# Optimization experiments

Hardware: AMD Instinct MI355X
Metric: run time of the kernel (lower is better)

The kernel has to match this reference:

```python
import jax, jax.numpy as jnp
import numpy as np

WS = 7            # window size
N = WS * WS       # tokens per window (49)
DIM = 128
HEADS = 4
HEAD_DIM = DIM // HEADS
SCALE = HEAD_DIM ** -0.5
NW = 64           # number of windows (mask leading dim)
B_WIN = 4096      # B * nW


def _relative_position_index():
    coords = np.stack(np.meshgrid(np.arange(WS), np.arange(WS), indexing='ij'))  # (2,WS,WS)
    cf = coords.reshape(2, -1)                       # (2, N)
    rel = cf[:, :, None] - cf[:, None, :]            # (2, N, N)
    rel = rel.transpose(1, 2, 0).copy()              # (N, N, 2)
    rel[..., 0] += WS - 1
    rel[..., 1] += WS - 1
    rel[..., 0] *= 2 * WS - 1
    return rel.sum(-1)                               # (N, N) int

REL_IDX = jnp.asarray(_relative_position_index())


def setup_inputs() -> dict:
    key = jax.random.key(0)
    ks = jax.random.split(key, 7)
    return {
        'x': jax.random.normal(ks[0], (B_WIN, N, DIM), dtype=jnp.float32),
        'mask': jax.random.normal(ks[1], (NW, N, N), dtype=jnp.float32),
        'qkv_w': jax.random.normal(ks[2], (3 * DIM, DIM), dtype=jnp.float32) * 0.02,
        'qkv_b': jax.random.normal(ks[3], (3 * DIM,), dtype=jnp.float32) * 0.02,
        'proj_w': jax.random.normal(ks[4], (DIM, DIM), dtype=jnp.float32) * 0.02,
        'proj_b': jax.random.normal(ks[5], (DIM,), dtype=jnp.float32) * 0.02,
        'bias_table': jax.random.normal(ks[6], ((2 * WS - 1) ** 2, HEADS), dtype=jnp.float32) * 0.02,
    }


def reference(x, mask, qkv_w, qkv_b, proj_w, proj_b, bias_table):
    B_, n, C = x.shape
    # qkv projection: (B_, N, 3C) -> (3, B_, H, N, hd)
    qkv = (x @ qkv_w.T + qkv_b).reshape(B_, n, 3, HEADS, HEAD_DIM)
    qkv = jnp.transpose(qkv, (2, 0, 3, 1, 4))
    q, k, v = qkv[0], qkv[1], qkv[2]
    # scaled scores: (B_, H, N, N)
    attn = jnp.einsum('bhnd,bhmd->bhnm', q * SCALE, k)
    # gathered relative position bias: (N, N, H) -> (H, N, N)
    rel_bias = jnp.transpose(bias_table[REL_IDX], (2, 0, 1))
    attn = attn + rel_bias[None]
    # shifted-window mask: broadcast over batch groups and heads
    nW = mask.shape[0]
    attn = attn.reshape(B_ // nW, nW, HEADS, n, n) + mask[None, :, None]
    attn = attn.reshape(B_, HEADS, n, n)
    attn = jax.nn.softmax(attn, axis=-1)
    out = jnp.einsum('bhnm,bhmd->bhnd', attn, v)
    out = jnp.transpose(out, (0, 2, 1, 3)).reshape(B_, n, C)
    return out @ proj_w.T + proj_b
```

## Files before the change

kernel.cpp:

```cpp
#include <hip/hip_runtime.h>

#define QK_SCALE 0.17677669529663687f

typedef __attribute__((ext_vector_type(8))) short bf16x8;
typedef __attribute__((ext_vector_type(4))) short bf16x4;
typedef __attribute__((ext_vector_type(4))) float floatx4;

__device__ __forceinline__ unsigned short f2bf(float f) {
    unsigned int u = __float_as_uint(f);
    u += 0x7fffu + ((u >> 16) & 1u);
    return (unsigned short)(u >> 16);
}

__device__ __forceinline__ bf16x8 ld8_2x4(const short* p) {
    union { bf16x8 v8; bf16x4 v4[2]; } u;
    u.v4[0] = *(const bf16x4*)p;
    u.v4[1] = *(const bf16x4*)(p + 4);
    return u.v8;
}

__global__ __launch_bounds__(256) void prep_kernel(
    const float* __restrict__ qkv_w, const float* __restrict__ proj_w,
    const float* __restrict__ bias_table, const float* __restrict__ mask,
    unsigned short* __restrict__ wbf, float* __restrict__ cm)
{
    int g = blockIdx.x * 256 + threadIdx.x;
    if (g < 49152) {
        wbf[g] = f2bf(qkv_w[g]);
    } else if (g < 65536) {
        wbf[g] = f2bf(proj_w[g - 49152]);
    } else if (g < 680192) {
        int t = g - 65536;
        int j = t % 49; int t2 = t / 49;
        int i = t2 % 49; int t3 = t2 / 49;
        int h = t3 & 3;  int wn = t3 >> 2;
        int idx = (i / 7 - j / 7 + 6) * 13 + (i % 7 - j % 7 + 6);
        cm[t] = mask[wn * 2401 + i * 49 + j] + bias_table[idx * 4 + h];
    }
}

__global__ __launch_bounds__(256, 3) void winattn_mfma(
    const float* __restrict__ x,
    const float* __restrict__ qkv_b,
    const float* __restrict__ proj_b,
    const unsigned short* __restrict__ wbf,
    const float* __restrict__ cm,
    float* __restrict__ out)
{
    __shared__ __align__(16) short smem[27136];

    const int tid  = threadIdx.x;
    const int lane = tid & 63;
    const int lid  = lane & 15;
    const int quad = lane >> 4;
    const int h    = tid >> 6;
    const int b    = blockIdx.x;
    const int w    = b & 63;
    const int hq   = h * 6784;

    {
        const float4* xg = (const float4*)(x + (size_t)b * 6272);
        for (int i = tid; i < 1568; i += 256) {
            int n = i >> 5, c4 = i & 31;
            float4 v = xg[i];
            ushort4 u;
            u.x = f2bf(v.x); u.y = f2bf(v.y); u.z = f2bf(v.z); u.w = f2bf(v.w);
            *(ushort4*)&smem[n * 136 + c4 * 4] = u;
        }
        ushort4 z; z.x = 0; z.y = 0; z.z = 0; z.w = 0;
        for (int i = tid; i < 510; i += 256)
            *(ushort4*)&smem[49 * 136 + i * 4] = z;
    }
    __syncthreads();

    bf16x8 ax[4][4];
    #pragma unroll
    for (int mt = 0; mt < 4; ++mt)
        #pragma unroll
        for (int kb = 0; kb < 4; ++kb)
            ax[mt][kb] = *(const bf16x8*)&smem[(mt * 16 + lid) * 136 + kb * 32 + quad * 8];
    __syncthreads();

    const floatx4 z4 = {0.f, 0.f, 0.f, 0.f};

    #pragma unroll
    for (int t = 0; t < 6; ++t) {
        const int cb = (t < 2) ? (h * 32 + t * 16)
                     : (t < 4) ? (128 + h * 32 + (t - 2) * 16)
                               : (256 + h * 32 + (t - 4) * 16);
        const unsigned short* wr = wbf + (size_t)(cb + lid) * 128 + quad * 8;
        floatx4 acc[4] = {z4, z4, z4, z4};
        #pragma unroll
        for (int kb = 0; kb < 4; ++kb) {
            bf16x8 bw = *(const bf16x8*)(wr + kb * 32);
            #pragma unroll
            for (int mt = 0; mt < 4; ++mt)
                acc[mt] = __builtin_amdgcn_mfma_f32_16x16x32_bf16(ax[mt][kb], bw, acc[mt], 0, 0, 0);
        }
        const float bias = qkv_b[cb + lid];
        #pragma unroll
        for (int mt = 0; mt < 4; ++mt) {
            #pragma unroll
            for (int r = 0; r < 4; ++r) {
                const int row = mt * 16 + quad * 4 + r;
                const float v = acc[mt][r] + bias;
                if (t < 2) {
                    smem[hq + row * 36 + t * 16 + lid] = (short)f2bf(v * QK_SCALE);
                } else if (t < 4) {
                    smem[hq + 2304 + row * 36 + (t - 2) * 16 + lid] = (short)f2bf(v);
                } else {
                    smem[hq + 4608 + ((t - 4) * 16 + lid) * 68 + row] = (short)f2bf(v);
                }
            }
        }
    }

    bf16x8 aq[4], bk[4];
    #pragma unroll
    for (int mt = 0; mt < 4; ++mt)
        aq[mt] = ld8_2x4(&smem[hq + (mt * 16 + lid) * 36 + quad * 8]);
    #pragma unroll
    for (int nt = 0; nt < 4; ++nt)
        bk[nt] = ld8_2x4(&smem[hq + 2304 + (nt * 16 + lid) * 36 + quad * 8]);

    floatx4 sacc[4][4];
    #pragma unroll
    for (int mt = 0; mt < 4; ++mt)
        #pragma unroll
        for (int nt = 0; nt < 4; ++nt)
            sacc[mt][nt] = __builtin_amdgcn_mfma_f32_16x16x32_bf16(aq[mt], bk[nt], z4, 0, 0, 0);

    float invs[4][4];
    const float* cmb = cm + (size_t)(w * 4 + h) * 2401;
    #pragma unroll
    for (int mt = 0; mt < 4; ++mt) {
        #pragma unroll
        for (int r = 0; r < 4; ++r) {
            const int row  = mt * 16 + quad * 4 + r;
            const int rowc = (row < 49) ? row : 48;
            float sv[4];
            #pragma unroll
            for (int nt = 0; nt < 4; ++nt) {
                const int col  = nt * 16 + lid;
                const int colc = (col < 49) ? col : 48;
                float val = sacc[mt][nt][r] + cmb[rowc * 49 + colc];
                sv[nt] = (col < 49) ? val : -1e30f;
            }
            float mx = fmaxf(fmaxf(sv[0], sv[1]), fmaxf(sv[2], sv[3]));
            #pragma unroll
            for (int d = 1; d < 16; d <<= 1) mx = fmaxf(mx, __shfl_xor(mx, d));
            float sum = 0.f;
            #pragma unroll
            for (int nt = 0; nt < 4; ++nt) { float p = __expf(sv[nt] - mx); sv[nt] = p; sum += p; }
            #pragma unroll
            for (int d = 1; d < 16; d <<= 1) sum += __shfl_xor(sum, d);
            invs[mt][r] = 1.f / sum;
            #pragma unroll
            for (int nt = 0; nt < 4; ++nt)
                smem[hq + row * 72 + nt * 16 + lid] = (short)f2bf(sv[nt]);
        }
    }

    bf16x8 bv[2][2];
    #pragma unroll
    for (int nt2 = 0; nt2 < 2; ++nt2)
        #pragma unroll
        for (int kb2 = 0; kb2 < 2; ++kb2)
            bv[nt2][kb2] = ld8_2x4(&smem[hq + 4608 + (nt2 * 16 + lid) * 68 + kb2 * 32 + quad * 8]);

    floatx4 oacc[4][2] = {{z4, z4}, {z4, z4}, {z4, z4}, {z4, z4}};
    #pragma unroll
    for (int mt = 0; mt < 4; ++mt) {
        #pragma unroll
        for (int kb2 = 0; kb2 < 2; ++kb2) {
            bf16x8 ap = *(const bf16x8*)&smem[hq + (mt * 16 + lid) * 72 + kb2 * 32 + quad * 8];
            #pragma unroll
            for (int nt2 = 0; nt2 < 2; ++nt2)
                oacc[mt][nt2] = __builtin_amdgcn_mfma_f32_16x16x32_bf16(ap, bv[nt2][kb2], oacc[mt][nt2], 0, 0, 0);
        }
    }

    __syncthreads();

    #pragma unroll
    for (int mt = 0; mt < 4; ++mt)
        #pragma unroll
        for (int nt2 = 0; nt2 < 2; ++nt2)
            #pragma unroll
            for (int r = 0; r < 4; ++r) {
                const int row = mt * 16 + quad * 4 + r;
                smem[row * 136 + h * 32 + nt2 * 16 + lid] =
                    (short)f2bf(oacc[mt][nt2][r] * invs[mt][r]);
            }
    __syncthreads();

    bf16x8 aa[4][4];
    #pragma unroll
    for (int mt = 0; mt < 4; ++mt)
        #pragma unroll
        for (int kb = 0; kb < 4; ++kb)
            aa[mt][kb] = *(const bf16x8*)&smem[(mt * 16 + lid) * 136 + kb * 32 + quad * 8];

    float* outb = out + (size_t)b * 6272;
    #pragma unroll
    for (int nt = 0; nt < 2; ++nt) {
        const int cb = h * 32 + nt * 16;
        const unsigned short* wr = wbf + 49152 + (size_t)(cb + lid) * 128 + quad * 8;
        floatx4 acc[4] = {z4, z4, z4, z4};
        #pragma unroll
        for (int kb = 0; kb < 4; ++kb) {
            bf16x8 bw = *(const bf16x8*)(wr + kb * 32);
            #pragma unroll
            for (int mt = 0; mt < 4; ++mt)
                acc[mt] = __builtin_amdgcn_mfma_f32_16x16x32_bf16(aa[mt][kb], bw, acc[mt], 0, 0, 0);
        }
        const float pb = proj_b[cb + lid];
        #pragma unroll
        for (int mt = 0; mt < 4; ++mt)
            #pragma unroll
            for (int r = 0; r < 4; ++r) {
                const int row = mt * 16 + quad * 4 + r;
                if (row < 49)
                    outb[row * 128 + cb + lid] = acc[mt][r] + pb;
            }
    }
}

extern "C" void kernel_launch(void* const* d_in, const int* in_sizes, int n_in,
                              void* d_out, int out_size, void* d_ws, size_t ws_size,
                              hipStream_t stream) {
    (void)in_sizes; (void)n_in; (void)out_size; (void)ws_size;
    const float* x          = (const float*)d_in[0];
    const float* mask       = (const float*)d_in[1];
    const float* qkv_w      = (const float*)d_in[2];
    const float* qkv_b      = (const float*)d_in[3];
    const float* proj_w     = (const float*)d_in[4];
    const float* proj_b     = (const float*)d_in[5];
    const float* bias_table = (const float*)d_in[6];

    unsigned short* wbf = (unsigned short*)d_ws;
    float* cm           = (float*)((char*)d_ws + 131072);

    prep_kernel<<<2657, 256, 0, stream>>>(qkv_w, proj_w, bias_table, mask, wbf, cm);
    winattn_mfma<<<4096, 256, 0, stream>>>(x, qkv_b, proj_b, wbf, cm, (float*)d_out);
}
```

Measured before the change: 300.5 us.

## Repack combined mask-bias into padded float4 layout and prefetch it per row tile

The prep kernel now writes the combined mask and relative-position bias in a layout padded to 64 columns, pre-filled with -1e30 for the padding, and interleaved so each lane reads its four column values as one float4. The attention kernel prefetches the next row tile of these values before doing the softmax on the current one, removing scalar clamped gathers and the column select. Shared-memory row strides are also tightened (36 to 34, 72 to 68), shrinking LDS use, which may allow more resident blocks. In exchange the prep kernel writes a somewhat larger table, and the odd strides need 2-element LDS loads.

```diff
diff --git a/kernel.cpp b/kernel.cpp
--- a/kernel.cpp
+++ b/kernel.cpp
@@ -4,6 +4,7 @@
 
 typedef __attribute__((ext_vector_type(8))) short bf16x8;
 typedef __attribute__((ext_vector_type(4))) short bf16x4;
+typedef __attribute__((ext_vector_type(2))) short bf16x2;
 typedef __attribute__((ext_vector_type(4))) float floatx4;
 
 __device__ __forceinline__ unsigned short f2bf(float f) {
@@ -19,23 +20,43 @@
     return u.v8;
 }
 
+__device__ __forceinline__ bf16x8 ld8_4x2(const short* p) {
+    union { bf16x8 v8; bf16x2 v2[4]; } u;
+    u.v2[0] = *(const bf16x2*)p;
+    u.v2[1] = *(const bf16x2*)(p + 2);
+    u.v2[2] = *(const bf16x2*)(p + 4);
+    u.v2[3] = *(const bf16x2*)(p + 6);
+    return u.v8;
+}
+
 __global__ __launch_bounds__(256) void prep_kernel(
     const float* __restrict__ qkv_w, const float* __restrict__ proj_w,
     const float* __restrict__ bias_table, const float* __restrict__ mask,
-    unsigned short* __restrict__ wbf, float* __restrict__ cm)
+    unsigned short* __restrict__ wbf, float* __restrict__ cm2)
 {
     int g = blockIdx.x * 256 + threadIdx.x;
     if (g < 49152) {
         wbf[g] = f2bf(qkv_w[g]);
     } else if (g < 65536) {
         wbf[g] = f2bf(proj_w[g - 49152]);
-    } else if (g < 680192) {
+    } else if (g < 868352) {
         int t = g - 65536;
-        int j = t % 49; int t2 = t / 49;
-        int i = t2 % 49; int t3 = t2 / 49;
-        int h = t3 & 3;  int wn = t3 >> 2;
-        int idx = (i / 7 - j / 7 + 6) * 13 + (i % 7 - j % 7 + 6);
-        cm[t] = mask[wn * 2401 + i * 49 + j] + bias_table[idx * 4 + h];
+        int nt  = t & 3;
+        int lid = (t >> 2) & 15;
+        int t2  = t >> 6;
+        int row = t2 % 49;
+        int wh  = t2 / 49;
+        int h   = wh & 3;
+        int w   = wh >> 2;
+        int col = nt * 16 + lid;
+        float v;
+        if (col < 49) {
+            int idx = (row / 7 - col / 7 + 6) * 13 + (row % 7 - col % 7 + 6);
+            v = mask[w * 2401 + row * 49 + col] + bias_table[idx * 4 + h];
+        } else {
+            v = -1e30f;
+        }
+        cm2[t] = v;
     }
 }
 
@@ -44,10 +65,10 @@
     const float* __restrict__ qkv_b,
     const float* __restrict__ proj_b,
     const unsigned short* __restrict__ wbf,
-    const float* __restrict__ cm,
+    const float* __restrict__ cm2,
     float* __restrict__ out)
 {
-    __shared__ __align__(16) short smem[27136];
+    __shared__ __align__(16) short smem[26112];
 
     const int tid  = threadIdx.x;
     const int lane = tid & 63;
@@ -56,7 +77,7 @@
     const int h    = tid >> 6;
     const int b    = blockIdx.x;
     const int w    = b & 63;
-    const int hq   = h * 6784;
+    const int hq   = h * 6528;
 
     {
         const float4* xg = (const float4*)(x + (size_t)b * 6272);
@@ -105,23 +126,29 @@
                 const int row = mt * 16 + quad * 4 + r;
                 const float v = acc[mt][r] + bias;
                 if (t < 2) {
-                    smem[hq + row * 36 + t * 16 + lid] = (short)f2bf(v * QK_SCALE);
+                    smem[hq + row * 34 + t * 16 + lid] = (short)f2bf(v * QK_SCALE);
                 } else if (t < 4) {
-                    smem[hq + 2304 + row * 36 + (t - 2) * 16 + lid] = (short)f2bf(v);
+                    smem[hq + 2176 + row * 34 + (t - 2) * 16 + lid] = (short)f2bf(v);
                 } else {
-                    smem[hq + 4608 + ((t - 4) * 16 + lid) * 68 + row] = (short)f2bf(v);
+                    smem[hq + 4352 + ((t - 4) * 16 + lid) * 68 + row] = (short)f2bf(v);
                 }
             }
         }
     }
 
+    const float4* cm2b = (const float4*)cm2 + ((size_t)(w * 4 + h) * 49) * 16 + lid;
+    float4 cmv[4][4];
+    #pragma unroll
+    for (int r = 0; r < 4; ++r)
+        cmv[0][r] = cm2b[(quad * 4 + r) * 16];
+
     bf16x8 aq[4], bk[4];
     #pragma unroll
     for (int mt = 0; mt < 4; ++mt)
-        aq[mt] = ld8_2x4(&smem[hq + (mt * 16 + lid) * 36 + quad * 8]);
+        aq[mt] = ld8_4x2(&smem[hq + (mt * 16 + lid) * 34 + quad * 8]);
     #pragma unroll
     for (int nt = 0; nt < 4; ++nt)
-        bk[nt] = ld8_2x4(&smem[hq + 2304 + (nt * 16 + lid) * 36 + quad * 8]);
+        bk[nt] = ld8_4x2(&smem[hq + 2176 + (nt * 16 + lid) * 34 + quad * 8]);
 
     floatx4 sacc[4][4];
     #pragma unroll
@@ -131,21 +158,23 @@
             sacc[mt][nt] = __builtin_amdgcn_mfma_f32_16x16x32_bf16(aq[mt], bk[nt], z4, 0, 0, 0);
 
     float invs[4][4];
-    const float* cmb = cm + (size_t)(w * 4 + h) * 2401;
     #pragma unroll
     for (int mt = 0; mt < 4; ++mt) {
+        if (mt < 3) {
+            #pragma unroll
+            for (int r = 0; r < 4; ++r) {
+                const int row  = (mt + 1) * 16 + quad * 4 + r;
+                const int rowc = (row < 49) ? row : 48;
+                cmv[mt + 1][r] = cm2b[rowc * 16];
+            }
+        }
         #pragma unroll
         for (int r = 0; r < 4; ++r) {
-            const int row  = mt * 16 + quad * 4 + r;
-            const int rowc = (row < 49) ? row : 48;
+            const int row = mt * 16 + quad * 4 + r;
             float sv[4];
             #pragma unroll
-            for (int nt = 0; nt < 4; ++nt) {
-                const int col  = nt * 16 + lid;
-                const int colc = (col < 49) ? col : 48;
-                float val = sacc[mt][nt][r] + cmb[rowc * 49 + colc];
-                sv[nt] = (col < 49) ? val : -1e30f;
-            }
+            for (int nt = 0; nt < 4; ++nt)
+                sv[nt] = sacc[mt][nt][r] + cmv[mt][r][nt];
             float mx = fmaxf(fmaxf(sv[0], sv[1]), fmaxf(sv[2], sv[3]));
             #pragma unroll
             for (int d = 1; d < 16; d <<= 1) mx = fmaxf(mx, __shfl_xor(mx, d));
@@ -157,7 +186,7 @@
             invs[mt][r] = 1.f / sum;
             #pragma unroll
             for (int nt = 0; nt < 4; ++nt)
-                smem[hq + row * 72 + nt * 16 + lid] = (short)f2bf(sv[nt]);
+                smem[hq + row * 68 + nt * 16 + lid] = (short)f2bf(sv[nt]);
         }
     }
 
@@ -166,14 +195,14 @@
     for (int nt2 = 0; nt2 < 2; ++nt2)
         #pragma unroll
         for (int kb2 = 0; kb2 < 2; ++kb2)
-            bv[nt2][kb2] = ld8_2x4(&smem[hq + 4608 + (nt2 * 16 + lid) * 68 + kb2 * 32 + quad * 8]);
+            bv[nt2][kb2] = ld8_2x4(&smem[hq + 4352 + (nt2 * 16 + lid) * 68 + kb2 * 32 + quad * 8]);
 
     floatx4 oacc[4][2] = {{z4, z4}, {z4, z4}, {z4, z4}, {z4, z4}};
     #pragma unroll
     for (int mt = 0; mt < 4; ++mt) {
         #pragma unroll
         for (int kb2 = 0; kb2 < 2; ++kb2) {
-            bf16x8 ap = *(const bf16x8*)&smem[hq + (mt * 16 + lid) * 72 + kb2 * 32 + quad * 8];
+            bf16x8 ap = ld8_2x4(&smem[hq + (mt * 16 + lid) * 68 + kb2 * 32 + quad * 8]);
             #pragma unroll
             for (int nt2 = 0; nt2 < 2; ++nt2)
                 oacc[mt][nt2] = __builtin_amdgcn_mfma_f32_16x16x32_bf16(ap, bv[nt2][kb2], oacc[mt][nt2], 0, 0, 0);
@@ -239,8 +268,8 @@
     const float* bias_table = (const float*)d_in[6];
 
     unsigned short* wbf = (unsigned short*)d_ws;
-    float* cm           = (float*)((char*)d_ws + 131072);
-
-    prep_kernel<<<2657, 256, 0, stream>>>(qkv_w, proj_w, bias_table, mask, wbf, cm);
-    winattn_mfma<<<4096, 256, 0, stream>>>(x, qkv_b, proj_b, wbf, cm, (float*)d_out);
-}
+    float* cm2          = (float*)((char*)d_ws + 131072);
+
+    prep_kernel<<<3392, 256, 0, stream>>>(qkv_w, proj_w, bias_table, mask, wbf, cm2);
+    winattn_mfma<<<4096, 256, 0, stream>>>(x, qkv_b, proj_b, wbf, cm2, (float*)d_out);
+}
```

Result: faster. 276.5 us (-8.0%).
